# Optimization experiments

Hardware: AMD Instinct MI355X
Metric: run time of the kernel (lower is better)

The kernel has to match this reference:

```python
import jax, jax.numpy as jnp
import numpy as np

EMBED_DIM = 1024
NUM_HEADS = 16
HEAD_DIM = EMBED_DIM // NUM_HEADS


def setup_inputs() -> dict:
    key = jax.random.key(0)
    ks = jax.random.split(key, 9)
    B, S, D = 2, 2048, EMBED_DIM
    scale = 1.0 / np.sqrt(D)
    x = jax.random.normal(ks[0], (B, S, D), dtype=jnp.float32)
    # Linear params (torch nn.Linear: y = x @ W.T + b); store W as [out, in]
    Wq = jax.random.normal(ks[1], (D, D), dtype=jnp.float32) * scale
    bq = jnp.zeros((D,), dtype=jnp.float32)
    Wk = jax.random.normal(ks[2], (D, D), dtype=jnp.float32) * scale
    bk = jnp.zeros((D,), dtype=jnp.float32)
    Wv = jax.random.normal(ks[3], (D, D), dtype=jnp.float32) * scale
    bv = jnp.zeros((D,), dtype=jnp.float32)
    Wo = jax.random.normal(ks[4], (D, D), dtype=jnp.float32) * scale
    bo = jnp.zeros((D,), dtype=jnp.float32)
    return {"x": x, "Wq": Wq, "bq": bq, "Wk": Wk, "bk": bk,
            "Wv": Wv, "bv": bv, "Wo": Wo, "bo": bo}


def reference(x, Wq, bq, Wk, bk, Wv, bv, Wo, bo):
    B, S, D = x.shape
    H, Hd = NUM_HEADS, HEAD_DIM
    scaling = Hd ** -0.5
    # projections (torch Linear: x @ W.T + b)
    q = (x @ Wq.T + bq).reshape(B, S, H, Hd).transpose(0, 2, 1, 3)  # [B,H,S,Hd]
    k = (x @ Wk.T + bk).reshape(B, S, H, Hd).transpose(0, 2, 1, 3)
    v = (x @ Wv.T + bv).reshape(B, S, H, Hd).transpose(0, 2, 1, 3)
    # full score matrix, as in the original (no flash tiling)
    scores = jnp.einsum('bhqd,bhkd->bhqk', q, k) * scaling  # [B,H,S,S]
    attn = jax.nn.softmax(scores, axis=-1)
    # dropout is identity in eval mode
    out = jnp.einsum('bhqk,bhkd->bhqd', attn, v)  # [B,H,S,Hd]
    out = out.transpose(0, 2, 1, 3).reshape(B, S, D)
    return out @ Wo.T + bo
```

## Files before the change

kernel.cpp:

```cpp
#include <hip/hip_runtime.h>
#include <stdint.h>

typedef unsigned short u16;
typedef short short8 __attribute__((ext_vector_type(8)));
typedef float f32x4 __attribute__((ext_vector_type(4)));
typedef float f32x16 __attribute__((ext_vector_type(16)));
typedef float f32x2 __attribute__((ext_vector_type(2)));

__device__ __forceinline__ u16 f2bf_fast(float f) {
  union { float f; uint32_t u; } x;
  x.f = f;
  return (u16)((x.u + 0x8000u) >> 16);
}

__device__ __forceinline__ uint32_t pack2bf(float lo, float hi) {
  union { float f; uint32_t u; } a, b;
  a.f = lo; b.f = hi;
  return __builtin_amdgcn_perm(b.u + 0x8000u, a.u + 0x8000u, 0x07060302u);
}

__device__ __forceinline__ float bf2f(uint32_t u) {
  union { uint32_t u; float f; } x;
  x.u = u << 16;
  return x.f;
}

__device__ __forceinline__ uint32_t cvtpk(float lo, float hi) {
  uint32_t r;
  asm("v_cvt_pk_bf16_f32 %0, %1, %2" : "=v"(r) : "v"(lo), "v"(hi));
  return r;
}

__device__ __forceinline__ void permswap(uint32_t& a, uint32_t& b) {
  asm("v_permlane32_swap_b32 %0, %1" : "+v"(a), "+v"(b));
}

__device__ __forceinline__ void gload_lds16(const void* g, void* l) {
  __builtin_amdgcn_global_load_lds(
      (const __attribute__((address_space(1))) void*)g,
      (__attribute__((address_space(3))) void*)l, 16, 0, 0);
}

__device__ __forceinline__ f32x4 mfma16(short8 a, short8 b, f32x4 c) {
  return __builtin_amdgcn_mfma_f32_16x16x32_bf16(a, b, c, 0, 0, 0);
}

__device__ __forceinline__ f32x16 mfma32(short8 a, short8 b, f32x16 c) {
  return __builtin_amdgcn_mfma_f32_32x32x16_bf16(a, b, c, 0, 0, 0);
}

#define QSCALE 0.18033688011112042f

__global__ void pack_all(const float* __restrict__ x, const float* __restrict__ wq,
                         const float* __restrict__ wk, const float* __restrict__ wv,
                         const float* __restrict__ wo, u16* __restrict__ xp,
                         u16* __restrict__ wp) {
  const int gi = blockIdx.x * 256 + threadIdx.x;
  const int lane = gi & 63;
  const int kc = (gi >> 6) & 31;
  const int rt = gi >> 11;
  const int col = kc * 32 + (lane >> 4) * 8;
  const float* src;
  int row;
  if (rt < 256) {
    src = x;
    row = rt * 16 + (lane & 15);
  } else {
    const int wti = rt - 256;
    const int widx = wti >> 6;
    src = (widx == 0) ? wq : (widx == 1) ? wk : (widx == 2) ? wv : wo;
    row = (wti & 63) * 16 + (lane & 15);
  }
  const float4* p = (const float4*)(src + (size_t)row * 1024 + col);
  const float4 v0 = p[0], v1 = p[1];
  uint4 o;
  o.x = pack2bf(v0.x, v0.y);
  o.y = pack2bf(v0.z, v0.w);
  o.z = pack2bf(v1.x, v1.y);
  o.w = pack2bf(v1.z, v1.w);
  u16* dst = (rt < 256) ? xp : wp;
  const int og = (rt < 256) ? gi : gi - 524288;
  ((uint4*)dst)[og] = o;
}

__global__ __launch_bounds__(256, 3) void proj_qkv(
    const u16* __restrict__ xp, const u16* __restrict__ wp,
    const float* __restrict__ bq, const float* __restrict__ bk,
    const float* __restrict__ bv, u16* __restrict__ qw, u16* __restrict__ kw,
    u16* __restrict__ vw) {
  __shared__ __align__(16) u16 As[8192];
  __shared__ __align__(16) u16 Bs[8192];
  const int tid = threadIdx.x, lane = tid & 63, w = tid >> 6;
  const int quad = lane >> 4, l15 = lane & 15;

  const int bid = blockIdx.x;
  const int work = (bid & 7) * 96 + (bid >> 3);
  const bool isQK = work < 512;
  int at0, bt0, bm2, bn2;
  const u16 *Ap, *Bp;
  if (isQK) {
    bm2 = work >> 4; bn2 = work & 15;
    Ap = xp; at0 = bm2 * 8;
    Bp = wp; bt0 = bn2 * 8;
  } else {
    const int h = work - 512;
    bm2 = h >> 5; bn2 = h & 31;
    Ap = wp; at0 = 128 + bm2 * 8;
    Bp = xp; bt0 = bn2 * 8;
  }
  const int wr = w >> 1, wc = w & 1;
  const int bm = bm2 * 2 + wr, bn = bn2 * 2 + wc;

  auto stage = [&](int kc, int buf) {
#pragma unroll
    for (int i = 0; i < 4; ++i) {
      const int g = w * 4 + i;
      const int t = g & 7;
      const u16* src = (g < 8)
          ? (Ap + (((at0 + t) << 5) + kc) * 512 + lane * 8)
          : (Bp + (((bt0 + t) << 5) + kc) * 512 + lane * 8);
      u16* dst = ((g < 8) ? As : Bs) + (buf * 8 + t) * 512 + lane * 8;
      gload_lds16(src, dst);
    }
  };

  f32x4 acc[4][4] = {};

  stage(0, 0);
  __syncthreads();

  for (int kc = 0; kc < 32; ++kc) {
    const int cur = kc & 1;
    if (kc < 31) stage(kc + 1, cur ^ 1);

    const u16* Ab = As + cur * 4096;
    const u16* Bb = Bs + cur * 4096;
    short8 af[4], bf[4];
#pragma unroll
    for (int mt = 0; mt < 4; ++mt)
      af[mt] = *(const short8*)&Ab[((wr * 4 + mt) * 64 + lane) * 8];
#pragma unroll
    for (int nt = 0; nt < 4; ++nt)
      bf[nt] = *(const short8*)&Bb[((wc * 4 + nt) * 64 + lane) * 8];

#pragma unroll
    for (int mt = 0; mt < 4; ++mt)
#pragma unroll
      for (int nt = 0; nt < 4; ++nt)
        acc[mt][nt] = mfma16(af[mt], bf[nt], acc[mt][nt]);
    __syncthreads();
  }

  u16* tw = ((w < 2) ? As : Bs) + (w & 1) * 4096;
#pragma unroll
  for (int nt = 0; nt < 4; ++nt) {
    const int n = bn * 64 + nt * 16 + l15;
    float ba = 0.f, sc = 1.f;
    if (isQK) {
      if (bn < 16) { ba = bq[n] * QSCALE; sc = QSCALE; }
      else          ba = bk[n - 1024];
    }
#pragma unroll
    for (int mt = 0; mt < 4; ++mt)
#pragma unroll
      for (int r = 0; r < 4; ++r) {
        const int m = bm * 64 + mt * 16 + quad * 4 + r;
        const float v = isQK ? (acc[mt][nt][r] * sc + ba)
                             : (acc[mt][nt][r] + bv[m]);
        tw[(mt * 16 + quad * 4 + r) * 64 + nt * 16 + l15] = f2bf_fast(v);
      }
  }
  const int rr = lane >> 3, ch = lane & 7;
  if (isQK) {
    const bool isQ = (bn < 16);
    u16* op = isQ ? qw : kw;
    const int hh = isQ ? bn : bn - 16;
#pragma unroll
    for (int p = 0; p < 8; ++p) {
      const int row = p * 8 + rr;
      const int m = bm * 64 + row;
      const int b = m >> 11, s = m & 2047;
      const uint4 val = *(const uint4*)&tw[row * 64 + ch * 8];
      *(uint4*)(op + ((size_t)((b * 16 + hh) * 2048 + s)) * 64 + ch * 8) = val;
    }
  } else {
    const int nb = bn * 64;
    const int b = nb >> 11, s = nb & 2047;
#pragma unroll
    for (int p = 0; p < 8; ++p) {
      const int row = p * 8 + rr;
      const int m = bm * 64 + row;
      const uint4 val = *(const uint4*)&tw[row * 64 + ch * 8];
      *(uint4*)(vw + ((size_t)(b * 1024 + m)) * 2048 + s + ch * 8) = val;
    }
  }
}

__global__ __launch_bounds__(512, 4) void attn_kernel(
    const u16* __restrict__ Q, const u16* __restrict__ Kt,
    const u16* __restrict__ Vt, u16* __restrict__ awp) {
  __shared__ __align__(16) u16 Sm[40960];
  const int tid = threadIdx.x, lane = tid & 63, w = tid >> 6;
  const int l31 = lane & 31, hi = lane >> 5, l7 = lane & 7;
  const int kh = w >> 2, qg = w & 3;

  const int bid = blockIdx.y * 16 + blockIdx.x;
  const int work = (bid & 7) * 64 + (bid >> 3);
  const int qt = work & 15;
  const int bh = work >> 4;

  const char* Qb = (const char*)(Q + ((size_t)bh * 2048 + qt * 128) * 64);
  const char* Kb = (const char*)(Kt + (size_t)bh * 2048 * 64);
  const char* Vb = (const char*)(Vt + (size_t)bh * 64 * 2048);

  auto stageKV = [&](int j, int buf) {
#pragma unroll
    for (int h = 0; h < 2; ++h) {
      const int kt = h * 16 + j;
      u16* Kl = Sm + (buf * 2 + h) * 8192;
      u16* Vl = Kl + 4096;
      const int G = w * 64 + lane;
      const int r = G >> 3, sl = G & 7;
      gload_lds16(Kb + (size_t)(kt * 64 + r) * 128 + ((sl ^ (r & 7)) * 16),
                  &Kl[G * 8]);
      gload_lds16(Vb + (size_t)r * 4096 + kt * 128 + ((sl ^ (r & 7)) * 16),
                  &Vl[G * 8]);
    }
  };

  u16* Qs = Sm + 32768;
#pragma unroll
  for (int i = 0; i < 2; ++i) {
    const int G = (w * 2 + i) * 64 + lane;
    const int row = G >> 3, sl = G & 7;
    gload_lds16(Qb + (size_t)row * 128 + ((sl ^ (row & 7)) * 16), &Qs[G * 8]);
  }
  stageKV(0, 0);
  __syncthreads();

  short8 aq[4];
#pragma unroll
  for (int ds = 0; ds < 4; ++ds)
    aq[ds] = *(const short8*)&Qs[(qg * 32 + l31) * 64 + (((ds << 1) + hi) ^ l7) * 8];

  f32x16 ot[2] = {};
  f32x2 l2 = {0.f, 0.f};

  for (int j = 0; j < 16; ++j) {
    const int buf = j & 1;
    if (j < 15) stageKV(j + 1, buf ^ 1);
    const u16* Kl = Sm + (buf * 2 + kh) * 8192;
    const u16* Vl = Kl + 4096;

#pragma unroll
    for (int t = 0; t < 2; ++t) {
      f32x16 st = {};
      __builtin_amdgcn_s_setprio(1);
#pragma unroll
      for (int ds = 0; ds < 4; ++ds) {
        short8 kf = *(const short8*)&Kl[(t * 32 + l31) * 64 +
                                        (((ds << 1) + hi) ^ l7) * 8];
        st = mfma32(kf, aq[ds], st);
      }
      __builtin_amdgcn_s_setprio(0);
      float e[16];
#pragma unroll
      for (int i = 0; i < 16; ++i) e[i] = __builtin_amdgcn_exp2f(st[i]);
#pragma unroll
      for (int i = 0; i < 8; ++i) l2 += (f32x2){e[2 * i], e[2 * i + 1]};

      uint32_t p01 = cvtpk(e[0], e[1]),   p23 = cvtpk(e[2], e[3]);
      uint32_t p45 = cvtpk(e[4], e[5]),   p67 = cvtpk(e[6], e[7]);
      uint32_t p89 = cvtpk(e[8], e[9]),   pAB = cvtpk(e[10], e[11]);
      uint32_t pCD = cvtpk(e[12], e[13]), pEF = cvtpk(e[14], e[15]);
      permswap(p01, p45);
      permswap(p23, p67);
      permswap(p89, pCD);
      permswap(pAB, pEF);
      union { uint32_t u[4]; short8 s; } b0, b1;
      b0.u[0] = p01; b0.u[1] = p23; b0.u[2] = p45; b0.u[3] = p67;
      b1.u[0] = p89; b1.u[1] = pAB; b1.u[2] = pCD; b1.u[3] = pEF;

      __builtin_amdgcn_s_setprio(1);
#pragma unroll
      for (int dt = 0; dt < 2; ++dt) {
#pragma unroll
        for (int s2 = 0; s2 < 2; ++s2) {
          short8 vf = *(const short8*)&Vl[(dt * 32 + l31) * 64 +
                                          ((((t * 2 + s2) << 1) + hi) ^ l7) * 8];
          ot[dt] = mfma32(vf, s2 ? b1.s : b0.s, ot[dt]);
        }
      }
      __builtin_amdgcn_s_setprio(0);
    }
    if (j < 15) __syncthreads();
  }

  float l = l2.x + l2.y;
  l += __shfl_xor(l, 32);

  __syncthreads();
  float* fb = (float*)Sm;
  if (kh == 1) {
    float* p = fb + (qg * 64 + lane) * 34;
#pragma unroll
    for (int i = 0; i < 8; ++i) {
      *(f32x2*)(p + 2 * i)      = (f32x2){ot[0][2 * i], ot[0][2 * i + 1]};
      *(f32x2*)(p + 16 + 2 * i) = (f32x2){ot[1][2 * i], ot[1][2 * i + 1]};
    }
    p[32] = l;
  }
  __syncthreads();
  if (kh == 0) {
    const float* p = fb + (qg * 64 + lane) * 34;
#pragma unroll
    for (int i = 0; i < 16; ++i) ot[0][i] += p[i];
#pragma unroll
    for (int i = 0; i < 16; ++i) ot[1][i] += p[16 + i];
    l += p[32];
    const float inv = __builtin_amdgcn_rcpf(l);

    const int b = bh >> 4, h = bh & 15;
    const int rt = b * 128 + qt * 8 + qg * 2 + (l31 >> 4);
#pragma unroll
    for (int dt = 0; dt < 2; ++dt) {
      const int kc = h * 2 + dt;
#pragma unroll
      for (int g = 0; g < 4; ++g) {
        const int ln = (lane & 15) + 16 * g;
        uint2 ov;
        ov.x = cvtpk(ot[dt][4 * g + 0] * inv, ot[dt][4 * g + 1] * inv);
        ov.y = cvtpk(ot[dt][4 * g + 2] * inv, ot[dt][4 * g + 3] * inv);
        *(uint2*)(awp + ((size_t)((rt * 32 + kc) * 64 + ln)) * 8 + hi * 4) = ov;
      }
    }
  }
}

__global__ __launch_bounds__(512, 2) void out_proj(const u16* __restrict__ awp,
                                                   const u16* __restrict__ wp,
                                                   const float* __restrict__ bo,
                                                   float* __restrict__ out) {
  __shared__ __align__(16) u16 As[8192];
  __shared__ __align__(16) u16 Bs[8192];
  const int tid = threadIdx.x, lane = tid & 63, w = tid >> 6;
  const int quad = lane >> 4, l15 = lane & 15;

  const int bid = blockIdx.x;
  const int work = (bid & 7) * 32 + (bid >> 3);
  const int bm2 = work >> 3, bn2 = work & 7;
  const int at0 = bm2 * 8, bt0 = 192 + bn2 * 8;
  const int wr = w >> 2, wc = w & 3;

  auto stage = [&](int kc, int buf) {
#pragma unroll
    for (int i = 0; i < 2; ++i) {
      const int g = w * 2 + i;
      const int t = g & 7;
      const u16* src = (g < 8)
          ? (awp + (((at0 + t) << 5) + kc) * 512 + lane * 8)
          : (wp + (((bt0 + t) << 5) + kc) * 512 + lane * 8);
      u16* dst = ((g < 8) ? As : Bs) + (buf * 8 + t) * 512 + lane * 8;
      gload_lds16(src, dst);
    }
  };

  f32x4 acc[4][2] = {};

  stage(0, 0);
  __syncthreads();

  for (int kc = 0; kc < 32; ++kc) {
    const int cur = kc & 1;
    if (kc < 31) stage(kc + 1, cur ^ 1);

    const u16* Ab = As + cur * 4096;
    const u16* Bb = Bs + cur * 4096;
    short8 af[4], bf[2];
#pragma unroll
    for (int mt = 0; mt < 4; ++mt)
      af[mt] = *(const short8*)&Ab[((wr * 4 + mt) * 64 + lane) * 8];
#pragma unroll
    for (int nt = 0; nt < 2; ++nt)
      bf[nt] = *(const short8*)&Bb[((wc * 2 + nt) * 64 + lane) * 8];

#pragma unroll
    for (int mt = 0; mt < 4; ++mt)
#pragma unroll
      for (int nt = 0; nt < 2; ++nt)
        acc[mt][nt] = mfma16(af[mt], bf[nt], acc[mt][nt]);
    __syncthreads();
  }

#pragma unroll
  for (int nt = 0; nt < 2; ++nt) {
    const int n = bn2 * 128 + wc * 32 + nt * 16 + l15;
    const float bb = bo[n];
#pragma unroll
    for (int mt = 0; mt < 4; ++mt)
#pragma unroll
      for (int r = 0; r < 4; ++r) {
        const int m = bm2 * 128 + wr * 64 + mt * 16 + quad * 4 + r;
        out[(size_t)m * 1024 + n] = acc[mt][nt][r] + bb;
      }
  }
}

extern "C" void kernel_launch(void* const* d_in, const int* in_sizes, int n_in,
                              void* d_out, int out_size, void* d_ws, size_t ws_size,
                              hipStream_t stream) {
  const float* x  = (const float*)d_in[0];
  const float* Wq = (const float*)d_in[1];
  const float* bq = (const float*)d_in[2];
  const float* Wk = (const float*)d_in[3];
  const float* bk = (const float*)d_in[4];
  const float* Wv = (const float*)d_in[5];
  const float* bv = (const float*)d_in[6];
  const float* Wo = (const float*)d_in[7];
  const float* bo = (const float*)d_in[8];

  const size_t M4 = (size_t)4 * 1024 * 1024;
  u16* xp  = (u16*)d_ws;
  u16* wp  = xp + M4;
  u16* qw  = wp + M4;
  u16* kw  = qw + M4;
  u16* vw  = kw + M4;
  u16* awp = vw + M4;

  pack_all<<<4096, 256, 0, stream>>>(x, Wq, Wk, Wv, Wo, xp, wp);

  proj_qkv<<<768, 256, 0, stream>>>(xp, wp, bq, bk, bv, qw, kw, vw);

  attn_kernel<<<dim3(16, 32), 512, 0, stream>>>(qw, kw, vw, awp);

  out_proj<<<256, 512, 0, stream>>>(awp, wp, bo, (float*)d_out);
}
```

Before: 180.2 us.

## Retile output projection to 128x64 blocks with doubled K-step per stage

Measured after the change: 175.9 us (median of 2 runs). -2.4%, faster.

```diff
diff --git a/kernel.cpp b/kernel.cpp
--- a/kernel.cpp
+++ b/kernel.cpp
@@ -337,70 +337,75 @@
   }
 }
 
-__global__ __launch_bounds__(512, 2) void out_proj(const u16* __restrict__ awp,
-                                                   const u16* __restrict__ wp,
-                                                   const float* __restrict__ bo,
-                                                   float* __restrict__ out) {
-  __shared__ __align__(16) u16 As[8192];
+__global__ __launch_bounds__(512) void out_proj(const u16* __restrict__ awp,
+                                                const u16* __restrict__ wp,
+                                                const float* __restrict__ bo,
+                                                float* __restrict__ out) {
+  __shared__ __align__(16) u16 As[16384];
   __shared__ __align__(16) u16 Bs[8192];
   const int tid = threadIdx.x, lane = tid & 63, w = tid >> 6;
   const int quad = lane >> 4, l15 = lane & 15;
 
   const int bid = blockIdx.x;
-  const int work = (bid & 7) * 32 + (bid >> 3);
-  const int bm2 = work >> 3, bn2 = work & 7;
-  const int at0 = bm2 * 8, bt0 = 192 + bn2 * 8;
-  const int wr = w >> 2, wc = w & 3;
-
-  auto stage = [&](int kc, int buf) {
+  const int work = (bid & 7) * 64 + (bid >> 3);
+  const int bm2 = work >> 4, bn2 = work & 15;
+  const int at0 = bm2 * 8, bt0 = 192 + bn2 * 4;
+  const int wr = w >> 1, wc = w & 1;
+
+  auto stage = [&](int ks, int buf) {
+    const int kc0 = ks * 2;
 #pragma unroll
     for (int i = 0; i < 2; ++i) {
-      const int g = w * 2 + i;
-      const int t = g & 7;
-      const u16* src = (g < 8)
-          ? (awp + (((at0 + t) << 5) + kc) * 512 + lane * 8)
-          : (wp + (((bt0 + t) << 5) + kc) * 512 + lane * 8);
-      u16* dst = ((g < 8) ? As : Bs) + (buf * 8 + t) * 512 + lane * 8;
+      const u16* src = awp + (((at0 + w) << 5) + kc0 + i) * 512 + lane * 8;
+      u16* dst = As + buf * 8192 + (i * 8 + w) * 512 + lane * 8;
       gload_lds16(src, dst);
     }
+    {
+      const int c = w >> 2, tg = w & 3;
+      const u16* src = wp + (((bt0 + tg) << 5) + kc0 + c) * 512 + lane * 8;
+      u16* dst = Bs + buf * 4096 + (c * 4 + tg) * 512 + lane * 8;
+      gload_lds16(src, dst);
+    }
   };
 
-  f32x4 acc[4][2] = {};
+  f32x4 acc[2][2] = {};
 
   stage(0, 0);
   __syncthreads();
 
-  for (int kc = 0; kc < 32; ++kc) {
-    const int cur = kc & 1;
-    if (kc < 31) stage(kc + 1, cur ^ 1);
-
-    const u16* Ab = As + cur * 4096;
+  for (int ks = 0; ks < 16; ++ks) {
+    const int cur = ks & 1;
+    if (ks < 15) stage(ks + 1, cur ^ 1);
+
+    const u16* Ab = As + cur * 8192;
     const u16* Bb = Bs + cur * 4096;
-    short8 af[4], bf[2];
-#pragma unroll
-    for (int mt = 0; mt < 4; ++mt)
-      af[mt] = *(const short8*)&Ab[((wr * 4 + mt) * 64 + lane) * 8];
-#pragma unroll
-    for (int nt = 0; nt < 2; ++nt)
-      bf[nt] = *(const short8*)&Bb[((wc * 2 + nt) * 64 + lane) * 8];
-
-#pragma unroll
-    for (int mt = 0; mt < 4; ++mt)
+#pragma unroll
+    for (int c = 0; c < 2; ++c) {
+      short8 af[2], bf[2];
+#pragma unroll
+      for (int mt = 0; mt < 2; ++mt)
+        af[mt] = *(const short8*)&Ab[((c * 8 + wr * 2 + mt) * 64 + lane) * 8];
 #pragma unroll
       for (int nt = 0; nt < 2; ++nt)
-        acc[mt][nt] = mfma16(af[mt], bf[nt], acc[mt][nt]);
+        bf[nt] = *(const short8*)&Bb[((c * 4 + wc * 2 + nt) * 64 + lane) * 8];
+#pragma unroll
+      for (int mt = 0; mt < 2; ++mt)
+#pragma unroll
+        for (int nt = 0; nt < 2; ++nt)
+          acc[mt][nt] = mfma16(af[mt], bf[nt], acc[mt][nt]);
+    }
     __syncthreads();
   }
 
 #pragma unroll
   for (int nt = 0; nt < 2; ++nt) {
-    const int n = bn2 * 128 + wc * 32 + nt * 16 + l15;
+    const int n = bn2 * 64 + wc * 32 + nt * 16 + l15;
     const float bb = bo[n];
 #pragma unroll
-    for (int mt = 0; mt < 4; ++mt)
+    for (int mt = 0; mt < 2; ++mt)
 #pragma unroll
       for (int r = 0; r < 4; ++r) {
-        const int m = bm2 * 128 + wr * 64 + mt * 16 + quad * 4 + r;
+        const int m = bm2 * 128 + wr * 32 + mt * 16 + quad * 4 + r;
         out[(size_t)m * 1024 + n] = acc[mt][nt][r] + bb;
       }
   }
@@ -433,5 +438,5 @@
 
   attn_kernel<<<dim3(16, 32), 512, 0, stream>>>(qw, kw, vw, awp);
 
-  out_proj<<<256, 512, 0, stream>>>(awp, wp, bo, (float*)d_out);
-}
+  out_proj<<<512, 512, 0, stream>>>(awp, wp, bo, (float*)d_out);
+}
```
